# Optimization experiments

Hardware: AMD Instinct MI355X
Metric: run time of the kernel (lower is better)

Reference implementation:

```python
import jax, jax.numpy as jnp
import numpy as np

EPS = 1e-6
NORM_FACTOR = 1000.0  # self.normalization_factor, aggregation 'sum'

# ---- Lorentz manifold (curvature -1, hyperboloid <x,x>_L = -1) ----

def _linner(x, y):
    # Lorentz inner product, keepdim on last axis
    return -x[..., :1] * y[..., :1] + jnp.sum(x[..., 1:] * y[..., 1:], axis=-1, keepdims=True)

def _proj_tan0(u):
    return jnp.concatenate([jnp.zeros_like(u[..., :1]), u[..., 1:]], axis=-1)

def _expmap0(u):
    sp = u[..., 1:]
    n = jnp.sqrt(jnp.clip(jnp.sum(sp * sp, axis=-1, keepdims=True), EPS))
    return jnp.concatenate([jnp.cosh(n), jnp.sinh(n) / n * sp], axis=-1)

def _logmap0(x):
    x0 = jnp.clip(x[..., :1], 1.0 + EPS)
    d = jnp.arccosh(x0)
    sp = x[..., 1:] * (d / jnp.sqrt(x0 * x0 - 1.0))
    return jnp.concatenate([jnp.zeros_like(x0), sp], axis=-1)

def _dist(x, y):
    return jnp.arccosh(jnp.clip(-_linner(x, y), 1.0 + EPS))

def _logmap(x, y):
    alpha = jnp.clip(-_linner(x, y), 1.0 + EPS)
    u = y - alpha * x                      # y + <x,y>_L x
    return jnp.arccosh(alpha) * u / jnp.sqrt(alpha * alpha - 1.0)

def _expmap(x, u):
    n = jnp.sqrt(jnp.clip(_linner(u, u), EPS))
    return jnp.cosh(n) * x + jnp.sinh(n) / n * u

def _proju(x, u):
    return u + _linner(x, u) * x

def _transp0(y, v):
    # parallel transport from origin o=(1,0,...,0) to y
    coef = _linner(y, v) / (1.0 + y[..., :1])
    oy = jnp.concatenate([y[..., :1] + 1.0, y[..., 1:]], axis=-1)
    return v + coef * oy

def _layernorm(x, g, b, eps=1e-5):
    m = jnp.mean(x, axis=-1, keepdims=True)
    v = jnp.mean((x - m) ** 2, axis=-1, keepdims=True)
    return (x - m) / jnp.sqrt(v + eps) * g + b


def setup_inputs() -> dict:
    N, E, D, ED = 10000, 320000, 128, 2
    key = jax.random.key(0)
    ks = jax.random.split(key, 10)
    # nodes on the hyperboloid: expmap0 of a small tangent vector
    h_tan = 0.02 * jax.random.normal(ks[0], (N, D), dtype=jnp.float32)
    h = _expmap0(_proj_tan0(h_tan))
    edge_attr = jax.random.normal(ks[1], (E, ED), dtype=jnp.float32)
    row = jax.random.randint(ks[2], (E,), 0, N, dtype=jnp.int32)
    col = jax.random.randint(ks[3], (E,), 0, N, dtype=jnp.int32)
    node_mask = jnp.ones((N, 1), dtype=jnp.float32)
    edge_mask = jnp.ones((E, 1), dtype=jnp.float32)
    s = 1.0 / np.sqrt(D)
    W = s * jax.random.normal(ks[4], (D, D), dtype=jnp.float32)
    bias = 0.0 * jax.random.normal(ks[5], (1, D), dtype=jnp.float32)  # init.constant_(bias, 0)
    att_in = 2 * D + ED + 1  # x_row, x_col, edge_attr + geodesic
    att_w1 = (1.0 / np.sqrt(att_in)) * jax.random.normal(ks[6], (att_in, D), dtype=jnp.float32)
    att_b1 = jnp.zeros((D,), dtype=jnp.float32)
    att_w2 = s * jax.random.normal(ks[7], (D, 1), dtype=jnp.float32)
    att_b2 = jnp.zeros((1,), dtype=jnp.float32)
    ln_gamma = jnp.ones((D - 1,), dtype=jnp.float32)
    ln_beta = jnp.zeros((D - 1,), dtype=jnp.float32)
    return {"h": h, "edge_attr": edge_attr, "row": row, "col": col,
            "node_mask": node_mask, "edge_mask": edge_mask, "W": W, "bias": bias,
            "att_w1": att_w1, "att_b1": att_b1, "att_w2": att_w2, "att_b2": att_b2,
            "ln_gamma": ln_gamma, "ln_beta": ln_beta}


def reference(h, edge_attr, row, col, node_mask, edge_mask, W, bias,
              att_w1, att_b1, att_w2, att_b2, ln_gamma, ln_beta):
    N = h.shape[0]
    # ---- HypLinear ----
    xt = _logmap0(h) @ W                  # Linear(in,out,bias=False)
    x = _expmap0(_proj_tan0(xt))
    b = _transp0(x, _proj_tan0(bias))
    x = _expmap(x, b)
    # ---- HypAgg ----
    x_tan = _logmap0(x)
    xr, xc = x[row], x[col]
    geo = _dist(xr, xc)                   # [E,1]
    att_in = jnp.concatenate([x_tan[row], x_tan[col], edge_attr, geo], axis=-1)
    hid = jax.nn.silu(att_in @ att_w1 + att_b1)
    att = jax.nn.sigmoid(hid @ att_w2 + att_b2) * edge_mask   # [E,1]
    loc = _logmap(xr, xc)                 # [E,D]
    agg = jax.ops.segment_sum(loc * att, row, num_segments=N) / NORM_FACTOR
    x = _expmap(x, _proju(x, agg))
    # ---- HNorm (Lorentz: LN on spatial components only) ----
    ht = _logmap0(x)
    sp = _layernorm(ht[..., 1:], ln_gamma, ln_beta)
    x = _expmap0(jnp.concatenate([ht[..., :1], sp], axis=-1))
    # ---- HypAct (manifold_out = Lorentz as well) ----
    xt = _proj_tan0(jax.nn.silu(_logmap0(x)))
    return _expmap0(xt)
```

## Files before the change

### kernel.cpp

```cpp
#include <hip/hip_runtime.h>
#include <math.h>

#define D 128
#define NPB 8
#define EPS1 (1.0f + 1e-6f)

__device__ __forceinline__ float dpp_rsum16(float v) {
    v += __int_as_float(__builtin_amdgcn_update_dpp(
        0, __float_as_int(v), 0x121, 0xf, 0xf, true));
    v += __int_as_float(__builtin_amdgcn_update_dpp(
        0, __float_as_int(v), 0x122, 0xf, 0xf, true));
    v += __int_as_float(__builtin_amdgcn_update_dpp(
        0, __float_as_int(v), 0x124, 0xf, 0xf, true));
    v += __int_as_float(__builtin_amdgcn_update_dpp(
        0, __float_as_int(v), 0x128, 0xf, 0xf, true));
    return v;
}

__device__ __forceinline__ float facosh(float a) {
    return __logf(a + sqrtf(fmaxf(a * a - 1.0f, 0.0f)));
}

__device__ __forceinline__ void unpack8(const float4& a, const float4& b,
                                        float* d) {
    d[0] = a.x; d[1] = a.y; d[2] = a.z; d[3] = a.w;
    d[4] = b.x; d[5] = b.y; d[6] = b.z; d[7] = b.w;
}

__device__ __forceinline__ void bsumH(float* v, float (*wred)[4], int lane,
                                      int wid, int kp) {
    __syncthreads();
#pragma unroll
    for (int o = 32; o; o >>= 1)
#pragma unroll
        for (int nl = 0; nl < 4; nl++) v[nl] += __shfl_xor(v[nl], o, 64);
    if (lane == 0)
#pragma unroll
        for (int nl = 0; nl < 4; nl++) wred[wid][nl] = v[nl];
    __syncthreads();
#pragma unroll
    for (int nl = 0; nl < 4; nl++)
        v[nl] = wred[2 * kp][nl] + wred[2 * kp + 1][nl];
}

__global__ __launch_bounds__(256) void node_pre8(
    const float* __restrict__ h, const float* __restrict__ W,
    const float* __restrict__ bias, const float* __restrict__ att_w1,
    const float* __restrict__ att_b1, float* __restrict__ XQ,
    float* __restrict__ P_out, const int* __restrict__ row,
    int* __restrict__ cnt, int N, int E) {
    int i0 = blockIdx.x * NPB;
    int tid = threadIdx.x;
    int j = tid & 127, kp = tid >> 7;
    int lane = tid & 63, wid = tid >> 6;
    int nbase = kp * 4;
    __shared__ __align__(16) float t8[NPB][D];
    __shared__ float psumP[2][NPB][D];
    __shared__ float psumQ[2][NPB][D];
    __shared__ float wred[4][4];

    float hj[4];
#pragma unroll
    for (int nl = 0; nl < 4; nl++) {
        int gi = i0 + nbase + nl;
        hj[nl] = (gi < N) ? h[(size_t)gi * D + j] : 0.0f;
        t8[nbase + nl][j] = hj[nl];
    }
    __syncthreads();
    float tj[4];
#pragma unroll
    for (int nl = 0; nl < 4; nl++) {
        float h0 = fmaxf(t8[nbase + nl][0], EPS1);
        float fac = facosh(h0) * rsqrtf(h0 * h0 - 1.0f);
        tj[nl] = (j == 0) ? 0.0f : hj[nl] * fac;
    }
    __syncthreads();
#pragma unroll
    for (int nl = 0; nl < 4; nl++) t8[nbase + nl][j] = tj[nl];
    __syncthreads();

    float xtp[NPB];
#pragma unroll
    for (int n = 0; n < NPB; n++) xtp[n] = 0.0f;
    int kbeg = kp * 64;
    for (int k0 = kbeg; k0 < kbeg + 64; k0 += 4) {
        float w0 = W[(k0 + 0) * D + j], w1 = W[(k0 + 1) * D + j];
        float w2 = W[(k0 + 2) * D + j], w3 = W[(k0 + 3) * D + j];
#pragma unroll
        for (int n = 0; n < NPB; n++) {
            float4 tv = *(const float4*)&t8[n][k0];
            xtp[n] = fmaf(tv.x, w0,
                          fmaf(tv.y, w1, fmaf(tv.z, w2, fmaf(tv.w, w3, xtp[n]))));
        }
    }
#pragma unroll
    for (int n = 0; n < NPB; n++) psumP[kp][n][j] = xtp[n];
    __syncthreads();
    float xt[4];
#pragma unroll
    for (int nl = 0; nl < 4; nl++) {
        int n = nbase + nl;
        xt[nl] = (j == 0) ? 0.0f : (psumP[0][n][j] + psumP[1][n][j]);
    }

    float v4[4];
#pragma unroll
    for (int nl = 0; nl < 4; nl++) v4[nl] = xt[nl] * xt[nl];
    bsumH(v4, wred, lane, wid, kp);
    float xj[4];
#pragma unroll
    for (int nl = 0; nl < 4; nl++) {
        float nn = sqrtf(fmaxf(v4[nl], 1e-6f));
        float e = __expf(nn), ei = __fdividef(1.0f, e);
        float ch = 0.5f * (e + ei), sh = 0.5f * (e - ei);
        xj[nl] = (j == 0) ? ch : __fdividef(sh, nn) * xt[nl];
    }

    float vj = (j == 0) ? 0.0f : bias[j];
#pragma unroll
    for (int nl = 0; nl < 4; nl++) v4[nl] = xj[nl] * vj;
    bsumH(v4, wred, lane, wid, kp);
    __syncthreads();
#pragma unroll
    for (int nl = 0; nl < 4; nl++) t8[nbase + nl][j] = xj[nl];
    __syncthreads();
    float bj[4];
#pragma unroll
    for (int nl = 0; nl < 4; nl++) {
        float X0 = t8[nbase + nl][0];
        float coef = __fdividef(v4[nl], 1.0f + X0);
        bj[nl] = vj + coef * ((j == 0) ? (X0 + 1.0f) : xj[nl]);
    }
#pragma unroll
    for (int nl = 0; nl < 4; nl++)
        v4[nl] = (j == 0) ? -bj[nl] * bj[nl] : bj[nl] * bj[nl];
    bsumH(v4, wred, lane, wid, kp);
    float xnj[4];
#pragma unroll
    for (int nl = 0; nl < 4; nl++) {
        float nb = sqrtf(fmaxf(v4[nl], 1e-6f));
        float e = __expf(nb), ei = __fdividef(1.0f, e);
        float ch = 0.5f * (e + ei), sh = 0.5f * (e - ei);
        xnj[nl] = ch * xj[nl] + __fdividef(sh, nb) * bj[nl];
        int gi = i0 + nbase + nl;
        if (gi < N) XQ[(size_t)gi * 256 + j] = xnj[nl];
    }

    __syncthreads();
#pragma unroll
    for (int nl = 0; nl < 4; nl++) t8[nbase + nl][j] = xnj[nl];
    __syncthreads();
    float xtj[4];
#pragma unroll
    for (int nl = 0; nl < 4; nl++) {
        float Y0 = fmaxf(t8[nbase + nl][0], EPS1);
        float f = facosh(Y0) * rsqrtf(Y0 * Y0 - 1.0f);
        xtj[nl] = (j == 0) ? 0.0f : xnj[nl] * f;
    }
    __syncthreads();
#pragma unroll
    for (int nl = 0; nl < 4; nl++) t8[nbase + nl][j] = xtj[nl];
    __syncthreads();

    float pp[NPB], qq[NPB];
#pragma unroll
    for (int n = 0; n < NPB; n++) {
        pp[n] = 0.0f;
        qq[n] = 0.0f;
    }
    for (int k0 = kbeg; k0 < kbeg + 64; k0 += 4) {
        float a0 = att_w1[(k0 + 0) * D + j], a1 = att_w1[(k0 + 1) * D + j];
        float a2 = att_w1[(k0 + 2) * D + j], a3 = att_w1[(k0 + 3) * D + j];
        float c0 = att_w1[(D + k0 + 0) * D + j], c1 = att_w1[(D + k0 + 1) * D + j];
        float c2 = att_w1[(D + k0 + 2) * D + j], c3 = att_w1[(D + k0 + 3) * D + j];
#pragma unroll
        for (int n = 0; n < NPB; n++) {
            float4 tv = *(const float4*)&t8[n][k0];
            pp[n] = fmaf(tv.x, a0,
                         fmaf(tv.y, a1, fmaf(tv.z, a2, fmaf(tv.w, a3, pp[n]))));
            qq[n] = fmaf(tv.x, c0,
                         fmaf(tv.y, c1, fmaf(tv.z, c2, fmaf(tv.w, c3, qq[n]))));
        }
    }
#pragma unroll
    for (int n = 0; n < NPB; n++) {
        psumP[kp][n][j] = pp[n];
        psumQ[kp][n][j] = qq[n];
    }
    __syncthreads();
    float b1 = att_b1[j];
#pragma unroll
    for (int nl = 0; nl < 4; nl++) {
        int n = nbase + nl;
        int gi = i0 + n;
        if (gi < N) {
            P_out[(size_t)gi * D + j] = psumP[0][n][j] + psumP[1][n][j] + b1;
            XQ[(size_t)gi * 256 + 128 + j] = psumQ[0][n][j] + psumQ[1][n][j];
        }
    }

    int gtid = blockIdx.x * 256 + tid;
    int tot = gridDim.x * 256;
    for (int e2 = gtid; e2 < E; e2 += tot) atomicAdd(&cnt[row[e2]], 1);
}

__global__ __launch_bounds__(1024) void scan_kernel(const int* __restrict__ cnt,
                                                    int* __restrict__ off,
                                                    int* __restrict__ cursor,
                                                    int N) {
    __shared__ int wsum[16];
    __shared__ int carry_s;
    int tid = threadIdx.x, lane = tid & 63, wid = tid >> 6;
    if (tid == 0) carry_s = 0;
    __syncthreads();
    for (int base = 0; base < N; base += 1024) {
        int idx = base + tid;
        int v = (idx < N) ? cnt[idx] : 0;
        int orig = v;
#pragma unroll
        for (int o = 1; o < 64; o <<= 1) {
            int t = __shfl_up(v, o, 64);
            if (lane >= o) v += t;
        }
        if (lane == 63) wsum[wid] = v;
        __syncthreads();
        if (wid == 0 && lane < 16) {
            int w = wsum[lane];
#pragma unroll
            for (int o = 1; o < 16; o <<= 1) {
                int t = __shfl_up(w, o, 64);
                if (lane >= o) w += t;
            }
            wsum[lane] = w;
        }
        __syncthreads();
        int carry = carry_s;
        int wbase = (wid == 0) ? 0 : wsum[wid - 1];
        int excl = carry + wbase + v - orig;
        if (idx < N) {
            off[idx] = excl;
            cursor[idx] = excl;
        }
        __syncthreads();
        if (tid == 1023) carry_s = carry + wsum[15];
        __syncthreads();
    }
}

__global__ void scatter_kernel(const int* __restrict__ row,
                               const int* __restrict__ col,
                               const float* __restrict__ edge_attr,
                               const float* __restrict__ edge_mask,
                               int* __restrict__ cursor,
                               float4* __restrict__ rec, int E) {
    const float2* ea2 = (const float2*)edge_attr;
    for (int e = blockIdx.x * blockDim.x + threadIdx.x; e < E;
         e += gridDim.x * blockDim.x) {
        int r = row[e];
        int pos = atomicAdd(&cursor[r], 1);
        float2 a = ea2[e];
        rec[pos] = make_float4(__int_as_float(col[e]), a.x, a.y, edge_mask[e]);
    }
}

__global__ __launch_bounds__(256) void edge_agg(
    const float* __restrict__ XQ, const float* __restrict__ P,
    const float4* __restrict__ rec, const int* __restrict__ off,
    const int* __restrict__ cnt, const float* __restrict__ w1c,
    const float* __restrict__ att_w2, const float* __restrict__ att_b2,
    const float* __restrict__ gamma, const float* __restrict__ beta,
    float* __restrict__ out, int N) {
    int tid = threadIdx.x, lane = tid & 63;
    int sub = lane & 15, grp = lane >> 4;
    int i = blockIdx.x * 4 + (tid >> 6);
    bool valid = i < N;
    i = min(i, N - 1);
    int j8 = sub * 8, f4 = sub * 2;

    const float4* w4 = (const float4*)w1c;
    const float4* aw4 = (const float4*)att_w2;
    const float4* xq4r = (const float4*)(XQ + (size_t)i * 256);
    const float4* pr4 = (const float4*)(P + (size_t)i * D);
    float xr[8], pr[8], wa[8], wb[8], wg[8], w2v[8];
    unpack8(xq4r[f4], xq4r[f4 + 1], xr);
    unpack8(pr4[f4], pr4[f4 + 1], pr);
    unpack8(w4[f4], w4[f4 + 1], wa);
    unpack8(w4[32 + f4], w4[32 + f4 + 1], wb);
    unpack8(w4[64 + f4], w4[64 + f4 + 1], wg);
    unpack8(aw4[f4], aw4[f4 + 1], w2v);
    float b2 = att_b2[0];
    float xr0s = (sub == 0) ? -xr[0] : xr[0];

    float acc[8];
#pragma unroll
    for (int u = 0; u < 8; u++) acc[u] = 0.0f;

    int s = off[i], m = valid ? cnt[i] : 0;
    int clen = (m + 3) >> 2;
    int k0 = grp * clen;
    int len = min(m, k0 + clen) - k0;

    auto compute = [&](const float4& rc, const float4& g0, const float4& g1,
                       const float4& g2, const float4& g3, bool act) {
        float xc[8], qc[8];
        unpack8(g0, g1, xc);
        unpack8(g2, g3, qc);
        float lin = xr0s * xc[0];
#pragma unroll
        for (int u = 1; u < 8; u++) lin = fmaf(xr[u], xc[u], lin);
        lin = dpp_rsum16(lin);
        float alpha = fmaxf(-lin, EPS1);
        float a2m = fmaxf(fmaf(alpha, alpha, -1.0f), 1e-12f);
        float rden = rsqrtf(a2m);
        float geo = __logf(fmaf(a2m, rden, alpha));
        float lp = 0.0f;
#pragma unroll
        for (int u = 0; u < 8; u++) {
            float hv = pr[u] + qc[u] +
                       fmaf(rc.y, wa[u], fmaf(rc.z, wb[u], geo * wg[u]));
            float sig = __fdividef(1.0f, 1.0f + __expf(-hv));
            lp = fmaf(hv * sig, w2v[u], lp);
        }
        lp = dpp_rsum16(lp);
        float w = act ? rc.w : 0.0f;
        float att = w * __fdividef(1.0f, 1.0f + __expf(-(lp + b2)));
        float scale = att * geo * rden * 1e-3f;
#pragma unroll
        for (int u = 0; u < 8; u++)
            acc[u] = fmaf(scale, fmaf(-alpha, xr[u], xc[u]), acc[u]);
    };

    float4 rcA = make_float4(__int_as_float(0), 0.0f, 0.0f, 0.0f), rcB;
    if (len > 0) rcA = rec[s + k0];
    const float4* pA =
        (const float4*)(XQ + (size_t)__float_as_int(rcA.x) * 256);
    float4 gA0 = pA[f4], gA1 = pA[f4 + 1], gA2 = pA[32 + f4],
           gA3 = pA[32 + f4 + 1];
    float4 gB0, gB1, gB2, gB3;

    for (int t = 0; t < clen; t += 2) {
        rcB = rcA;
        if (t + 1 < len) rcB = rec[s + k0 + t + 1];
        const float4* pB =
            (const float4*)(XQ + (size_t)__float_as_int(rcB.x) * 256);
        gB0 = pB[f4]; gB1 = pB[f4 + 1]; gB2 = pB[32 + f4]; gB3 = pB[32 + f4 + 1];
        compute(rcA, gA0, gA1, gA2, gA3, t < len);
        rcA = rcB;
        if (t + 2 < len) rcA = rec[s + k0 + t + 2];
        const float4* pN =
            (const float4*)(XQ + (size_t)__float_as_int(rcA.x) * 256);
        gA0 = pN[f4]; gA1 = pN[f4 + 1]; gA2 = pN[32 + f4]; gA3 = pN[32 + f4 + 1];
        compute(rcB, gB0, gB1, gB2, gB3, t + 1 < len);
    }

#pragma unroll
    for (int u = 0; u < 8; u++) {
        acc[u] += __shfl_xor(acc[u], 16, 64);
        acc[u] += __shfl_xor(acc[u], 32, 64);
    }

    float lxa_p = (sub == 0) ? -xr[0] * acc[0] : xr[0] * acc[0];
#pragma unroll
    for (int u = 1; u < 8; u++) lxa_p = fmaf(xr[u], acc[u], lxa_p);
    float lxa = dpp_rsum16(lxa_p);
    float uj[8];
#pragma unroll
    for (int u = 0; u < 8; u++) uj[u] = fmaf(lxa, xr[u], acc[u]);
    float luu_p = (sub == 0) ? -uj[0] * uj[0] : uj[0] * uj[0];
#pragma unroll
    for (int u = 1; u < 8; u++) luu_p = fmaf(uj[u], uj[u], luu_p);
    float luu = dpp_rsum16(luu_p);
    float nn = sqrtf(fmaxf(luu, 1e-6f));
    float e = __expf(nn), ei = __fdividef(1.0f, e);
    float ch = 0.5f * (e + ei), shv = __fdividef(0.5f * (e - ei), nn);
    float xn[8];
#pragma unroll
    for (int u = 0; u < 8; u++) xn[u] = ch * xr[u] + shv * uj[u];
    float X0 = __shfl(xn[0], lane & 48, 64);
    X0 = fmaxf(X0, EPS1);
    float fc = facosh(X0) * rsqrtf(X0 * X0 - 1.0f);
    float ht[8];
#pragma unroll
    for (int u = 0; u < 8; u++) ht[u] = xn[u] * fc;
    if (sub == 0) ht[0] = 0.0f;
    float mp = 0.0f;
#pragma unroll
    for (int u = 0; u < 8; u++) mp += ht[u];
    float mean = dpp_rsum16(mp) * (1.0f / 127.0f);
    float diff[8];
#pragma unroll
    for (int u = 0; u < 8; u++) diff[u] = ht[u] - mean;
    if (sub == 0) diff[0] = 0.0f;
    float vp = 0.0f;
#pragma unroll
    for (int u = 0; u < 8; u++) vp = fmaf(diff[u], diff[u], vp);
    float var = dpp_rsum16(vp) * (1.0f / 127.0f);
    float rstd = rsqrtf(var + 1e-5f);
    float sp[8];
#pragma unroll
    for (int u = 0; u < 8; u++) {
        int j = j8 + u;
        sp[u] = (j > 0) ? fmaf(diff[u] * rstd, gamma[j - 1], beta[j - 1]) : 0.0f;
    }
    float n2p = 0.0f;
#pragma unroll
    for (int u = 0; u < 8; u++) n2p = fmaf(sp[u], sp[u], n2p);
    float n2 = sqrtf(fmaxf(dpp_rsum16(n2p), 1e-6f));
    e = __expf(n2);
    ei = __fdividef(1.0f, e);
    float y0 = 0.5f * (e + ei), sh2 = __fdividef(0.5f * (e - ei), n2);
    float yj[8];
#pragma unroll
    for (int u = 0; u < 8; u++) yj[u] = sh2 * sp[u];
    if (sub == 0) yj[0] = y0;
    float y0c = fmaxf(y0, EPS1);
    float f3 = facosh(y0c) * rsqrtf(y0c * y0c - 1.0f);
    float sj[8];
#pragma unroll
    for (int u = 0; u < 8; u++) {
        float lj = yj[u] * f3;
        sj[u] = __fdividef(lj, 1.0f + __expf(-lj));
    }
    if (sub == 0) sj[0] = 0.0f;
    float n3p = 0.0f;
#pragma unroll
    for (int u = 0; u < 8; u++) n3p = fmaf(sj[u], sj[u], n3p);
    float n3 = sqrtf(fmaxf(dpp_rsum16(n3p), 1e-6f));
    e = __expf(n3);
    ei = __fdividef(1.0f, e);
    float o0 = 0.5f * (e + ei), sh3 = __fdividef(0.5f * (e - ei), n3);
    float ov[8];
#pragma unroll
    for (int u = 0; u < 8; u++) ov[u] = sh3 * sj[u];
    if (sub == 0) ov[0] = o0;
    if (valid && grp == 0) {
        float4* o4 = (float4*)(out + (size_t)i * D);
        o4[f4] = make_float4(ov[0], ov[1], ov[2], ov[3]);
        o4[f4 + 1] = make_float4(ov[4], ov[5], ov[6], ov[7]);
    }
}

extern "C" void kernel_launch(void* const* d_in, const int* in_sizes, int n_in,
                              void* d_out, int out_size, void* d_ws,
                              size_t ws_size, hipStream_t stream) {
    const float* h = (const float*)d_in[0];
    const float* edge_attr = (const float*)d_in[1];
    const int* row = (const int*)d_in[2];
    const int* col = (const int*)d_in[3];
    const float* edge_mask = (const float*)d_in[5];
    const float* W = (const float*)d_in[6];
    const float* bias = (const float*)d_in[7];
    const float* att_w1 = (const float*)d_in[8];
    const float* att_b1 = (const float*)d_in[9];
    const float* att_w2 = (const float*)d_in[10];
    const float* att_b2 = (const float*)d_in[11];
    const float* ln_g = (const float*)d_in[12];
    const float* ln_b = (const float*)d_in[13];

    int N = in_sizes[0] / D;
    int E = in_sizes[2];

    float* XQ = (float*)d_ws;
    float* Pbuf = XQ + (size_t)N * 256;
    float4* rec = (float4*)(Pbuf + (size_t)N * D);
    int* cnt = (int*)(rec + E);
    int* off = cnt + N;
    int* cur = off + N;

    hipMemsetAsync(cnt, 0, N * sizeof(int), stream);
    node_pre8<<<(N + NPB - 1) / NPB, 256, 0, stream>>>(
        h, W, bias, att_w1, att_b1, XQ, Pbuf, row, cnt, N, E);
    scan_kernel<<<1, 1024, 0, stream>>>(cnt, off, cur, N);
    scatter_kernel<<<640, 256, 0, stream>>>(row, col, edge_attr, edge_mask,
                                            cur, rec, E);
    edge_agg<<<(N + 3) / 4, 256, 0, stream>>>(XQ, Pbuf, rec, off, cnt,
                                              att_w1 + 256 * D, att_w2, att_b2,
                                              ln_g, ln_b, (float*)d_out, N);
}
```

Measured before the change: 146.4 us.

## Restructure node pre-kernel per-wavefront, single-pass scan, hoist LayerNorm params

The node preprocessing kernel now assigns four nodes to each wavefront, with two output columns per lane. Row norms become wavefront-wide DPP/shuffle reductions, which removes most block-level __syncthreads and the shared partial-sum buffers, and each block covers 16 nodes. The scan kernel changes from a looping chunked scan with several barriers per chunk to one pass where each thread scans a contiguous segment. The edge kernel hoists the gamma/beta loads out of the epilogue. The trade-off is that weight rows are now read per wavefront rather than shared across the block, and the scan's local array caps at 16 entries per thread (N up to 16384).

```diff
diff --git a/kernel.cpp b/kernel.cpp
--- a/kernel.cpp
+++ b/kernel.cpp
@@ -2,7 +2,6 @@
 #include <math.h>
 
 #define D 128
-#define NPB 8
 #define EPS1 (1.0f + 1e-6f)
 
 __device__ __forceinline__ float dpp_rsum16(float v) {
@@ -17,6 +16,13 @@
     return v;
 }
 
+__device__ __forceinline__ float wsum64(float v) {
+    v = dpp_rsum16(v);
+    v += __shfl_xor(v, 16, 64);
+    v += __shfl_xor(v, 32, 64);
+    return v;
+}
+
 __device__ __forceinline__ float facosh(float a) {
     return __logf(a + sqrtf(fmaxf(a * a - 1.0f, 0.0f)));
 }
@@ -27,175 +33,135 @@
     d[4] = b.x; d[5] = b.y; d[6] = b.z; d[7] = b.w;
 }
 
-__device__ __forceinline__ void bsumH(float* v, float (*wred)[4], int lane,
-                                      int wid, int kp) {
-    __syncthreads();
-#pragma unroll
-    for (int o = 32; o; o >>= 1)
-#pragma unroll
-        for (int nl = 0; nl < 4; nl++) v[nl] += __shfl_xor(v[nl], o, 64);
-    if (lane == 0)
-#pragma unroll
-        for (int nl = 0; nl < 4; nl++) wred[wid][nl] = v[nl];
-    __syncthreads();
-#pragma unroll
-    for (int nl = 0; nl < 4; nl++)
-        v[nl] = wred[2 * kp][nl] + wred[2 * kp + 1][nl];
-}
-
-__global__ __launch_bounds__(256) void node_pre8(
+__global__ __launch_bounds__(256) void node_pre16(
     const float* __restrict__ h, const float* __restrict__ W,
     const float* __restrict__ bias, const float* __restrict__ att_w1,
     const float* __restrict__ att_b1, float* __restrict__ XQ,
     float* __restrict__ P_out, const int* __restrict__ row,
     int* __restrict__ cnt, int N, int E) {
-    int i0 = blockIdx.x * NPB;
-    int tid = threadIdx.x;
-    int j = tid & 127, kp = tid >> 7;
-    int lane = tid & 63, wid = tid >> 6;
-    int nbase = kp * 4;
-    __shared__ __align__(16) float t8[NPB][D];
-    __shared__ float psumP[2][NPB][D];
-    __shared__ float psumQ[2][NPB][D];
-    __shared__ float wred[4][4];
-
-    float hj[4];
-#pragma unroll
-    for (int nl = 0; nl < 4; nl++) {
-        int gi = i0 + nbase + nl;
-        hj[nl] = (gi < N) ? h[(size_t)gi * D + j] : 0.0f;
-        t8[nbase + nl][j] = hj[nl];
-    }
-    __syncthreads();
-    float tj[4];
-#pragma unroll
-    for (int nl = 0; nl < 4; nl++) {
-        float h0 = fmaxf(t8[nbase + nl][0], EPS1);
-        float fac = facosh(h0) * rsqrtf(h0 * h0 - 1.0f);
-        tj[nl] = (j == 0) ? 0.0f : hj[nl] * fac;
-    }
-    __syncthreads();
-#pragma unroll
-    for (int nl = 0; nl < 4; nl++) t8[nbase + nl][j] = tj[nl];
-    __syncthreads();
-
-    float xtp[NPB];
-#pragma unroll
-    for (int n = 0; n < NPB; n++) xtp[n] = 0.0f;
-    int kbeg = kp * 64;
-    for (int k0 = kbeg; k0 < kbeg + 64; k0 += 4) {
-        float w0 = W[(k0 + 0) * D + j], w1 = W[(k0 + 1) * D + j];
-        float w2 = W[(k0 + 2) * D + j], w3 = W[(k0 + 3) * D + j];
-#pragma unroll
-        for (int n = 0; n < NPB; n++) {
-            float4 tv = *(const float4*)&t8[n][k0];
-            xtp[n] = fmaf(tv.x, w0,
-                          fmaf(tv.y, w1, fmaf(tv.z, w2, fmaf(tv.w, w3, xtp[n]))));
-        }
-    }
-#pragma unroll
-    for (int n = 0; n < NPB; n++) psumP[kp][n][j] = xtp[n];
-    __syncthreads();
-    float xt[4];
-#pragma unroll
-    for (int nl = 0; nl < 4; nl++) {
-        int n = nbase + nl;
-        xt[nl] = (j == 0) ? 0.0f : (psumP[0][n][j] + psumP[1][n][j]);
-    }
-
-    float v4[4];
-#pragma unroll
-    for (int nl = 0; nl < 4; nl++) v4[nl] = xt[nl] * xt[nl];
-    bsumH(v4, wred, lane, wid, kp);
-    float xj[4];
-#pragma unroll
-    for (int nl = 0; nl < 4; nl++) {
-        float nn = sqrtf(fmaxf(v4[nl], 1e-6f));
+    int tid = threadIdx.x, lane = tid & 63, wv = tid >> 6;
+    int base = blockIdx.x * 16 + wv * 4;
+    int j0 = 2 * lane;
+    __shared__ __align__(16) float ts[16][D];
+
+    int gi[4];
+    bool val[4];
+#pragma unroll
+    for (int n = 0; n < 4; n++) {
+        val[n] = base + n < N;
+        gi[n] = min(base + n, N - 1);
+    }
+
+    float ta[4], tb[4];
+#pragma unroll
+    for (int n = 0; n < 4; n++) {
+        float2 h2 = *(const float2*)&h[(size_t)gi[n] * D + j0];
+        float h0 = __shfl(h2.x, 0, 64);
+        float h0c = fmaxf(h0, EPS1);
+        float fac = facosh(h0c) * rsqrtf(h0c * h0c - 1.0f);
+        ta[n] = (lane == 0) ? 0.0f : h2.x * fac;
+        tb[n] = h2.y * fac;
+        *(float2*)&ts[wv * 4 + n][j0] = make_float2(ta[n], tb[n]);
+    }
+
+    float xta[4] = {0, 0, 0, 0}, xtb[4] = {0, 0, 0, 0};
+    for (int k0 = 0; k0 < D; k0 += 4) {
+        float4 tv0 = *(const float4*)&ts[wv * 4 + 0][k0];
+        float4 tv1 = *(const float4*)&ts[wv * 4 + 1][k0];
+        float4 tv2 = *(const float4*)&ts[wv * 4 + 2][k0];
+        float4 tv3 = *(const float4*)&ts[wv * 4 + 3][k0];
+        float2 w0 = *(const float2*)&W[(k0 + 0) * D + j0];
+        float2 w1 = *(const float2*)&W[(k0 + 1) * D + j0];
+        float2 w2 = *(const float2*)&W[(k0 + 2) * D + j0];
+        float2 w3 = *(const float2*)&W[(k0 + 3) * D + j0];
+        xta[0] = fmaf(tv0.x, w0.x, fmaf(tv0.y, w1.x, fmaf(tv0.z, w2.x, fmaf(tv0.w, w3.x, xta[0]))));
+        xtb[0] = fmaf(tv0.x, w0.y, fmaf(tv0.y, w1.y, fmaf(tv0.z, w2.y, fmaf(tv0.w, w3.y, xtb[0]))));
+        xta[1] = fmaf(tv1.x, w0.x, fmaf(tv1.y, w1.x, fmaf(tv1.z, w2.x, fmaf(tv1.w, w3.x, xta[1]))));
+        xtb[1] = fmaf(tv1.x, w0.y, fmaf(tv1.y, w1.y, fmaf(tv1.z, w2.y, fmaf(tv1.w, w3.y, xtb[1]))));
+        xta[2] = fmaf(tv2.x, w0.x, fmaf(tv2.y, w1.x, fmaf(tv2.z, w2.x, fmaf(tv2.w, w3.x, xta[2]))));
+        xtb[2] = fmaf(tv2.x, w0.y, fmaf(tv2.y, w1.y, fmaf(tv2.z, w2.y, fmaf(tv2.w, w3.y, xtb[2]))));
+        xta[3] = fmaf(tv3.x, w0.x, fmaf(tv3.y, w1.x, fmaf(tv3.z, w2.x, fmaf(tv3.w, w3.x, xta[3]))));
+        xtb[3] = fmaf(tv3.x, w0.y, fmaf(tv3.y, w1.y, fmaf(tv3.z, w2.y, fmaf(tv3.w, w3.y, xtb[3]))));
+    }
+    if (lane == 0)
+#pragma unroll
+        for (int n = 0; n < 4; n++) xta[n] = 0.0f;
+
+    float2 bv = *(const float2*)&bias[j0];
+    float va = (lane == 0) ? 0.0f : bv.x, vb = bv.y;
+    float xna[4], xnb[4];
+#pragma unroll
+    for (int n = 0; n < 4; n++) {
+        float nsq = wsum64(xta[n] * xta[n] + xtb[n] * xtb[n]);
+        float nn = sqrtf(fmaxf(nsq, 1e-6f));
         float e = __expf(nn), ei = __fdividef(1.0f, e);
-        float ch = 0.5f * (e + ei), sh = 0.5f * (e - ei);
-        xj[nl] = (j == 0) ? ch : __fdividef(sh, nn) * xt[nl];
-    }
-
-    float vj = (j == 0) ? 0.0f : bias[j];
-#pragma unroll
-    for (int nl = 0; nl < 4; nl++) v4[nl] = xj[nl] * vj;
-    bsumH(v4, wred, lane, wid, kp);
-    __syncthreads();
-#pragma unroll
-    for (int nl = 0; nl < 4; nl++) t8[nbase + nl][j] = xj[nl];
-    __syncthreads();
-    float bj[4];
-#pragma unroll
-    for (int nl = 0; nl < 4; nl++) {
-        float X0 = t8[nbase + nl][0];
-        float coef = __fdividef(v4[nl], 1.0f + X0);
-        bj[nl] = vj + coef * ((j == 0) ? (X0 + 1.0f) : xj[nl]);
-    }
-#pragma unroll
-    for (int nl = 0; nl < 4; nl++)
-        v4[nl] = (j == 0) ? -bj[nl] * bj[nl] : bj[nl] * bj[nl];
-    bsumH(v4, wred, lane, wid, kp);
-    float xnj[4];
-#pragma unroll
-    for (int nl = 0; nl < 4; nl++) {
-        float nb = sqrtf(fmaxf(v4[nl], 1e-6f));
-        float e = __expf(nb), ei = __fdividef(1.0f, e);
-        float ch = 0.5f * (e + ei), sh = 0.5f * (e - ei);
-        xnj[nl] = ch * xj[nl] + __fdividef(sh, nb) * bj[nl];
-        int gi = i0 + nbase + nl;
-        if (gi < N) XQ[(size_t)gi * 256 + j] = xnj[nl];
-    }
-
-    __syncthreads();
-#pragma unroll
-    for (int nl = 0; nl < 4; nl++) t8[nbase + nl][j] = xnj[nl];
-    __syncthreads();
-    float xtj[4];
-#pragma unroll
-    for (int nl = 0; nl < 4; nl++) {
-        float Y0 = fmaxf(t8[nbase + nl][0], EPS1);
-        float f = facosh(Y0) * rsqrtf(Y0 * Y0 - 1.0f);
-        xtj[nl] = (j == 0) ? 0.0f : xnj[nl] * f;
-    }
-    __syncthreads();
-#pragma unroll
-    for (int nl = 0; nl < 4; nl++) t8[nbase + nl][j] = xtj[nl];
-    __syncthreads();
-
-    float pp[NPB], qq[NPB];
-#pragma unroll
-    for (int n = 0; n < NPB; n++) {
-        pp[n] = 0.0f;
-        qq[n] = 0.0f;
-    }
-    for (int k0 = kbeg; k0 < kbeg + 64; k0 += 4) {
-        float a0 = att_w1[(k0 + 0) * D + j], a1 = att_w1[(k0 + 1) * D + j];
-        float a2 = att_w1[(k0 + 2) * D + j], a3 = att_w1[(k0 + 3) * D + j];
-        float c0 = att_w1[(D + k0 + 0) * D + j], c1 = att_w1[(D + k0 + 1) * D + j];
-        float c2 = att_w1[(D + k0 + 2) * D + j], c3 = att_w1[(D + k0 + 3) * D + j];
-#pragma unroll
-        for (int n = 0; n < NPB; n++) {
-            float4 tv = *(const float4*)&t8[n][k0];
-            pp[n] = fmaf(tv.x, a0,
-                         fmaf(tv.y, a1, fmaf(tv.z, a2, fmaf(tv.w, a3, pp[n]))));
-            qq[n] = fmaf(tv.x, c0,
-                         fmaf(tv.y, c1, fmaf(tv.z, c2, fmaf(tv.w, c3, qq[n]))));
-        }
-    }
-#pragma unroll
-    for (int n = 0; n < NPB; n++) {
-        psumP[kp][n][j] = pp[n];
-        psumQ[kp][n][j] = qq[n];
-    }
-    __syncthreads();
-    float b1 = att_b1[j];
-#pragma unroll
-    for (int nl = 0; nl < 4; nl++) {
-        int n = nbase + nl;
-        int gi = i0 + n;
-        if (gi < N) {
-            P_out[(size_t)gi * D + j] = psumP[0][n][j] + psumP[1][n][j] + b1;
-            XQ[(size_t)gi * 256 + 128 + j] = psumQ[0][n][j] + psumQ[1][n][j];
+        float ch = 0.5f * (e + ei), sh = __fdividef(0.5f * (e - ei), nn);
+        float xa = (lane == 0) ? ch : sh * xta[n];
+        float xb = sh * xtb[n];
+        float lxv = wsum64(xa * va + xb * vb);
+        float coef = __fdividef(lxv, 1.0f + ch);
+        float ba = (lane == 0) ? coef * (ch + 1.0f) : fmaf(coef, xa, va);
+        float bb = fmaf(coef, xb, vb);
+        float lbb = wsum64(((lane == 0) ? -ba * ba : ba * ba) + bb * bb);
+        float nb = sqrtf(fmaxf(lbb, 1e-6f));
+        float e2 = __expf(nb), ei2 = __fdividef(1.0f, e2);
+        float ch2 = 0.5f * (e2 + ei2), sh2 = __fdividef(0.5f * (e2 - ei2), nb);
+        xna[n] = ch2 * xa + sh2 * ba;
+        xnb[n] = ch2 * xb + sh2 * bb;
+        if (val[n])
+            *(float2*)&XQ[(size_t)gi[n] * 256 + j0] = make_float2(xna[n], xnb[n]);
+    }
+
+#pragma unroll
+    for (int n = 0; n < 4; n++) {
+        float Y0 = __shfl(xna[n], 0, 64);
+        float Y0c = fmaxf(Y0, EPS1);
+        float f = facosh(Y0c) * rsqrtf(Y0c * Y0c - 1.0f);
+        float xta2 = (lane == 0) ? 0.0f : xna[n] * f;
+        float xtb2 = xnb[n] * f;
+        *(float2*)&ts[wv * 4 + n][j0] = make_float2(xta2, xtb2);
+    }
+
+    float pa[4] = {0, 0, 0, 0}, pb[4] = {0, 0, 0, 0};
+    float qa[4] = {0, 0, 0, 0}, qb[4] = {0, 0, 0, 0};
+    for (int k0 = 0; k0 < D; k0 += 4) {
+        float4 tv0 = *(const float4*)&ts[wv * 4 + 0][k0];
+        float4 tv1 = *(const float4*)&ts[wv * 4 + 1][k0];
+        float4 tv2 = *(const float4*)&ts[wv * 4 + 2][k0];
+        float4 tv3 = *(const float4*)&ts[wv * 4 + 3][k0];
+        float2 a0 = *(const float2*)&att_w1[(k0 + 0) * D + j0];
+        float2 a1 = *(const float2*)&att_w1[(k0 + 1) * D + j0];
+        float2 a2 = *(const float2*)&att_w1[(k0 + 2) * D + j0];
+        float2 a3 = *(const float2*)&att_w1[(k0 + 3) * D + j0];
+        float2 c0 = *(const float2*)&att_w1[(D + k0 + 0) * D + j0];
+        float2 c1 = *(const float2*)&att_w1[(D + k0 + 1) * D + j0];
+        float2 c2 = *(const float2*)&att_w1[(D + k0 + 2) * D + j0];
+        float2 c3 = *(const float2*)&att_w1[(D + k0 + 3) * D + j0];
+        pa[0] = fmaf(tv0.x, a0.x, fmaf(tv0.y, a1.x, fmaf(tv0.z, a2.x, fmaf(tv0.w, a3.x, pa[0]))));
+        pb[0] = fmaf(tv0.x, a0.y, fmaf(tv0.y, a1.y, fmaf(tv0.z, a2.y, fmaf(tv0.w, a3.y, pb[0]))));
+        qa[0] = fmaf(tv0.x, c0.x, fmaf(tv0.y, c1.x, fmaf(tv0.z, c2.x, fmaf(tv0.w, c3.x, qa[0]))));
+        qb[0] = fmaf(tv0.x, c0.y, fmaf(tv0.y, c1.y, fmaf(tv0.z, c2.y, fmaf(tv0.w, c3.y, qb[0]))));
+        pa[1] = fmaf(tv1.x, a0.x, fmaf(tv1.y, a1.x, fmaf(tv1.z, a2.x, fmaf(tv1.w, a3.x, pa[1]))));
+        pb[1] = fmaf(tv1.x, a0.y, fmaf(tv1.y, a1.y, fmaf(tv1.z, a2.y, fmaf(tv1.w, a3.y, pb[1]))));
+        qa[1] = fmaf(tv1.x, c0.x, fmaf(tv1.y, c1.x, fmaf(tv1.z, c2.x, fmaf(tv1.w, c3.x, qa[1]))));
+        qb[1] = fmaf(tv1.x, c0.y, fmaf(tv1.y, c1.y, fmaf(tv1.z, c2.y, fmaf(tv1.w, c3.y, qb[1]))));
+        pa[2] = fmaf(tv2.x, a0.x, fmaf(tv2.y, a1.x, fmaf(tv2.z, a2.x, fmaf(tv2.w, a3.x, pa[2]))));
+        pb[2] = fmaf(tv2.x, a0.y, fmaf(tv2.y, a1.y, fmaf(tv2.z, a2.y, fmaf(tv2.w, a3.y, pb[2]))));
+        qa[2] = fmaf(tv2.x, c0.x, fmaf(tv2.y, c1.x, fmaf(tv2.z, c2.x, fmaf(tv2.w, c3.x, qa[2]))));
+        qb[2] = fmaf(tv2.x, c0.y, fmaf(tv2.y, c1.y, fmaf(tv2.z, c2.y, fmaf(tv2.w, c3.y, qb[2]))));
+        pa[3] = fmaf(tv3.x, a0.x, fmaf(tv3.y, a1.x, fmaf(tv3.z, a2.x, fmaf(tv3.w, a3.x, pa[3]))));
+        pb[3] = fmaf(tv3.x, a0.y, fmaf(tv3.y, a1.y, fmaf(tv3.z, a2.y, fmaf(tv3.w, a3.y, pb[3]))));
+        qa[3] = fmaf(tv3.x, c0.x, fmaf(tv3.y, c1.x, fmaf(tv3.z, c2.x, fmaf(tv3.w, c3.x, qa[3]))));
+        qb[3] = fmaf(tv3.x, c0.y, fmaf(tv3.y, c1.y, fmaf(tv3.z, c2.y, fmaf(tv3.w, c3.y, qb[3]))));
+    }
+    float2 b1v = *(const float2*)&att_b1[j0];
+#pragma unroll
+    for (int n = 0; n < 4; n++) {
+        if (val[n]) {
+            *(float2*)&P_out[(size_t)gi[n] * D + j0] =
+                make_float2(pa[n] + b1v.x, pb[n] + b1v.y);
+            *(float2*)&XQ[(size_t)gi[n] * 256 + 128 + j0] =
+                make_float2(qa[n], qb[n]);
         }
     }
 
@@ -208,42 +174,46 @@
                                                     int* __restrict__ off,
                                                     int* __restrict__ cursor,
                                                     int N) {
-    __shared__ int wsum[16];
-    __shared__ int carry_s;
+    __shared__ int wt[16];
     int tid = threadIdx.x, lane = tid & 63, wid = tid >> 6;
-    if (tid == 0) carry_s = 0;
+    int PER = (N + 1023) >> 10;
+    int basei = tid * PER;
+    int loc[16];
+    int tsum = 0;
+#pragma unroll 4
+    for (int r = 0; r < PER; r++) {
+        int idx = basei + r;
+        int v = (idx < N) ? cnt[idx] : 0;
+        loc[r] = tsum;
+        tsum += v;
+    }
+    int inc = tsum;
+#pragma unroll
+    for (int o = 1; o < 64; o <<= 1) {
+        int t = __shfl_up(inc, o, 64);
+        if (lane >= o) inc += t;
+    }
+    if (lane == 63) wt[wid] = inc;
     __syncthreads();
-    for (int base = 0; base < N; base += 1024) {
-        int idx = base + tid;
-        int v = (idx < N) ? cnt[idx] : 0;
-        int orig = v;
-#pragma unroll
-        for (int o = 1; o < 64; o <<= 1) {
-            int t = __shfl_up(v, o, 64);
-            if (lane >= o) v += t;
+    if (tid < 16) {
+        int w = wt[tid];
+#pragma unroll
+        for (int o = 1; o < 16; o <<= 1) {
+            int t = __shfl_up(w, o, 64);
+            if ((tid & 15) >= o) w += t;
         }
-        if (lane == 63) wsum[wid] = v;
-        __syncthreads();
-        if (wid == 0 && lane < 16) {
-            int w = wsum[lane];
-#pragma unroll
-            for (int o = 1; o < 16; o <<= 1) {
-                int t = __shfl_up(w, o, 64);
-                if (lane >= o) w += t;
-            }
-            wsum[lane] = w;
+        wt[tid] = w;
+    }
+    __syncthreads();
+    int wbase = (wid == 0) ? 0 : wt[wid - 1];
+    int texcl = wbase + inc - tsum;
+    for (int r = 0; r < PER; r++) {
+        int idx = basei + r;
+        if (idx < N) {
+            int o = texcl + loc[r];
+            off[idx] = o;
+            cursor[idx] = o;
         }
-        __syncthreads();
-        int carry = carry_s;
-        int wbase = (wid == 0) ? 0 : wsum[wid - 1];
-        int excl = carry + wbase + v - orig;
-        if (idx < N) {
-            off[idx] = excl;
-            cursor[idx] = excl;
-        }
-        __syncthreads();
-        if (tid == 1023) carry_s = carry + wsum[15];
-        __syncthreads();
     }
 }
 
@@ -290,6 +260,13 @@
     unpack8(aw4[f4], aw4[f4 + 1], w2v);
     float b2 = att_b2[0];
     float xr0s = (sub == 0) ? -xr[0] : xr[0];
+    float g_ln[8], bt_ln[8];
+#pragma unroll
+    for (int u = 0; u < 8; u++) {
+        int j = j8 + u;
+        g_ln[u] = (j > 0) ? gamma[j - 1] : 0.0f;
+        bt_ln[u] = (j > 0) ? beta[j - 1] : 0.0f;
+    }
 
     float acc[8];
 #pragma unroll
@@ -343,13 +320,15 @@
         if (t + 1 < len) rcB = rec[s + k0 + t + 1];
         const float4* pB =
             (const float4*)(XQ + (size_t)__float_as_int(rcB.x) * 256);
-        gB0 = pB[f4]; gB1 = pB[f4 + 1]; gB2 = pB[32 + f4]; gB3 = pB[32 + f4 + 1];
+        gB0 = pB[f4]; gB1 = pB[f4 + 1]; gB2 = pB[32 + f4];
+        gB3 = pB[32 + f4 + 1];
         compute(rcA, gA0, gA1, gA2, gA3, t < len);
         rcA = rcB;
         if (t + 2 < len) rcA = rec[s + k0 + t + 2];
         const float4* pN =
             (const float4*)(XQ + (size_t)__float_as_int(rcA.x) * 256);
-        gA0 = pN[f4]; gA1 = pN[f4 + 1]; gA2 = pN[32 + f4]; gA3 = pN[32 + f4 + 1];
+        gA0 = pN[f4]; gA1 = pN[f4 + 1]; gA2 = pN[32 + f4];
+        gA3 = pN[32 + f4 + 1];
         compute(rcB, gB0, gB1, gB2, gB3, t + 1 < len);
     }
 
@@ -398,10 +377,9 @@
     float rstd = rsqrtf(var + 1e-5f);
     float sp[8];
 #pragma unroll
-    for (int u = 0; u < 8; u++) {
-        int j = j8 + u;
-        sp[u] = (j > 0) ? fmaf(diff[u] * rstd, gamma[j - 1], beta[j - 1]) : 0.0f;
-    }
+    for (int u = 0; u < 8; u++)
+        sp[u] = fmaf(diff[u] * rstd, g_ln[u], bt_ln[u]);
+    if (sub == 0) sp[0] = 0.0f;
     float n2p = 0.0f;
 #pragma unroll
     for (int u = 0; u < 8; u++) n2p = fmaf(sp[u], sp[u], n2p);
@@ -468,7 +446,7 @@
     int* cur = off + N;
 
     hipMemsetAsync(cnt, 0, N * sizeof(int), stream);
-    node_pre8<<<(N + NPB - 1) / NPB, 256, 0, stream>>>(
+    node_pre16<<<(N + 15) / 16, 256, 0, stream>>>(
         h, W, bias, att_w1, att_b1, XQ, Pbuf, row, cnt, N, E);
     scan_kernel<<<1, 1024, 0, stream>>>(cnt, off, cur, N);
     scatter_kernel<<<640, 256, 0, stream>>>(row, col, edge_attr, edge_mask,
```

New measurement: 154.2 us. 1.05x slower.
